# Kernel optimization log

Measured on AMD Instinct MI355X. Metric: run time of the kernel, lower is better.

## Reference

```python
import jax, jax.numpy as jnp
import numpy as np

B, N, D = 128, 64, 2048   # batch, num_slots, slot_dim
M, K, C = 8, 4096, 256    # num_codebooks, codebook_size, code_dim
BLK = D // M              # block size per codebook = 256
COMMIT = 0.25


def setup_inputs() -> dict:
    key = jax.random.key(0)
    ks = jax.random.split(key, 5)
    return {
        "slots": jax.random.normal(ks[0], (B, N, D), dtype=jnp.float32),
        # per-codebook input projections: Linear(BLK -> C), stacked over M
        "Wp": jax.random.normal(ks[1], (M, BLK, C), dtype=jnp.float32) * (1.0 / np.sqrt(BLK)),
        "bp": jnp.zeros((M, C), dtype=jnp.float32),
        # M codebooks of K codes each, uniform(-1/K, 1/K) like the torch init
        "codebooks": jax.random.uniform(ks[2], (M, K, C), dtype=jnp.float32, minval=-1.0 / K, maxval=1.0 / K),
        # per-codebook output projections: Linear(C -> BLK)
        "Wo": jax.random.normal(ks[3], (M, C, BLK), dtype=jnp.float32) * (1.0 / np.sqrt(C)),
        "bo": jnp.zeros((M, BLK), dtype=jnp.float32),
    }


def reference(slots, Wp, bp, codebooks, Wo, bo):
    # split slots into M blocks: [B, N, M, BLK]
    blocks = slots.reshape(B, N, M, BLK)
    # per-codebook projection -> [B, N, M, C]
    x = jnp.einsum('bnmd,mdc->bnmc', blocks, Wp) + bp
    # squared-euclidean distances to each code: [B, N, M, K]
    dist = (jnp.sum(x * x, axis=-1, keepdims=True)
            + jnp.sum(codebooks * codebooks, axis=-1)[None, None]  # [M, K]
            - 2.0 * jnp.einsum('bnmc,mkc->bnmk', x, codebooks))
    idx = jnp.argmin(dist, axis=-1)                 # [B, N, M] int
    # gather codes: codebooks[m, idx[b,n,m]] -> [B, N, M, C]
    q = codebooks[jnp.arange(M)[None, None, :], idx]
    # VQ loss: per-codebook mse summed then / M == global mean over [B,N,M,C]
    q_loss = jnp.mean((q - jax.lax.stop_gradient(x)) ** 2)
    e_loss = jnp.mean((jax.lax.stop_gradient(q) - x) ** 2)
    loss = q_loss + COMMIT * e_loss
    # straight-through estimator
    q_st = x + jax.lax.stop_gradient(q - x)
    # per-codebook output projection and concat of blocks -> [B, N, D]
    out = jnp.einsum('bnmc,mcd->bnmd', q_st, Wo) + bo
    return out.reshape(B, N, D), loss, idx
```

## Files before the change

### kernel.cpp

```cpp
#include <hip/hip_runtime.h>
#include <hip/hip_bf16.h>

typedef float f32x4 __attribute__((ext_vector_type(4)));
typedef float f32x2 __attribute__((ext_vector_type(2)));
typedef short bf16x8 __attribute__((ext_vector_type(8)));

static constexpr size_t WS_LOSSP = 0;
static constexpr size_t WS_UMIN  = 16384;
static constexpr size_t WS_B32   = 294912;
static constexpr size_t WS_IDX   = 425984;
static constexpr size_t WS_CNT   = 688128;
static constexpr size_t WS_LST   = 950272;
static constexpr size_t WS_XH    = 3145728;
static constexpr size_t WS_CBT   = 70254592;

#define DELTA 3.0e-4f

__device__ inline unsigned int fkey(float f) {
  unsigned int b = __float_as_uint(f); return (b & 0x80000000u) ? ~b : (b | 0x80000000u);
}
__device__ inline float funkey(unsigned int u) {
  unsigned int b = (u & 0x80000000u) ? (u ^ 0x80000000u) : ~u; return __uint_as_float(b);
}

__device__ inline f32x2 pk_mul(f32x2 a, f32x2 b) {
  f32x2 d;
  asm("v_pk_mul_f32 %0, %1, %2" : "=v"(d) : "v"(a), "v"(b));
  return d;
}
__device__ inline f32x2 pk_add(f32x2 a, f32x2 b) {
  f32x2 d;
  asm("v_pk_add_f32 %0, %1, %2" : "=v"(d) : "v"(a), "v"(b));
  return d;
}

__device__ inline float np_pw256sq(const float* p, int stride) {
#pragma clang fp contract(off)
  float h2[2];
#pragma unroll
  for (int hh = 0; hh < 2; ++hh) {
    const float* q = p + (size_t)(hh * 128) * stride;
    float V[16];
#pragma unroll
    for (int i = 0; i < 16; ++i) {
      float e[8];
#pragma unroll
      for (int j = 0; j < 8; ++j) { float x = q[(size_t)(j * 16 + i) * stride]; e[j] = x * x; }
      float t01 = e[0] + e[1], t23 = e[2] + e[3], t45 = e[4] + e[5], t67 = e[6] + e[7];
      float ta = t01 + t23, tb = t45 + t67;
      V[i] = ta + tb;
    }
    float u[8];
#pragma unroll
    for (int i = 0; i < 8; ++i) u[i] = V[i] + V[8 + i];
    float w[4];
#pragma unroll
    for (int i = 0; i < 4; ++i) w[i] = u[i] + u[4 + i];
    float wa = w[0] + w[2], wb = w[1] + w[3];
    h2[hh] = wa + wb;
  }
  return h2[0] + h2[1];
}

__global__ __launch_bounds__(256) void k_cbnormB(const float* __restrict__ cb,
                                                 float* __restrict__ B32) {
  int row = blockIdx.x * 256 + threadIdx.x;
  B32[row] = np_pw256sq(cb + (size_t)row * 256, 1);
}

__global__ __launch_bounds__(256) void k_cbb(const float* __restrict__ cb,
                                             unsigned short* __restrict__ cbb) {
  int bx = blockIdx.x;
  int m = bx >> 8, kt = bx & 255;
  const float* src = cb + ((size_t)m * 4096 + kt * 16) * 256;
  unsigned short* dst = cbb + ((size_t)(m * 256 + kt)) * 4096;
  int tid = threadIdx.x;
#pragma unroll
  for (int h = 0; h < 2; ++h) {
    int p = tid + h * 256;
    int cs = p >> 6, lane = p & 63, row = lane & 15, grp = lane >> 4;
    const float* s = src + (size_t)row * 256 + grp * 8 + cs * 32;
    f32x4 v0 = *(const f32x4*)s;
    f32x4 v1 = *(const f32x4*)(s + 4);
    union { unsigned short us[8]; uint4 u; } o;
#pragma unroll
    for (int j = 0; j < 4; ++j) {
      __hip_bfloat16 h0 = __float2bfloat16(v0[j]);
      __hip_bfloat16 h1 = __float2bfloat16(v1[j]);
      o.us[j]     = *reinterpret_cast<unsigned short*>(&h0);
      o.us[4 + j] = *reinterpret_cast<unsigned short*>(&h1);
    }
    *(uint4*)(dst + (size_t)p * 8) = o.u;
  }
}

__global__ __launch_bounds__(256) void k_xhat(const float* __restrict__ slots,
                                              const float* __restrict__ Wp,
                                              const float* __restrict__ bp,
                                              float* __restrict__ XH) {
#pragma clang fp contract(off)
  int bx = blockIdx.x;
  int m = bx & 7, tt = bx >> 3;
  int t0 = tt * 16;
  __shared__ float Ls[16 * 260];
  __shared__ float Wt[16 * 264];
  int tid = threadIdx.x;
  {
#pragma unroll
    for (int i = 0; i < 4; ++i) {
      int f = tid + 256 * i;
      int r = f >> 6, seg = f & 63;
      *(f32x4*)&Ls[r * 260 + seg * 4] =
          *(const f32x4*)(slots + (size_t)(t0 + r) * 2048 + m * 256 + seg * 4);
    }
  }
  int tl = tid & 15, g = tid >> 4;
  const float* lsrow = &Ls[tl * 260];
  const f32x4* wglob = (const f32x4*)(Wp + (size_t)m * 65536);
  f32x4 preg[4];
#pragma unroll
  for (int i = 0; i < 4; ++i) preg[i] = wglob[tid + 256 * i];

  f32x2 acc[8];
#pragma unroll
  for (int i = 0; i < 8; ++i) acc[i] = f32x2{0.f, 0.f};

  for (int chunk = 0; chunk < 16; ++chunk) {
    __syncthreads();
    {
      f32x4* wt4 = (f32x4*)Wt;
#pragma unroll
      for (int i = 0; i < 4; ++i) {
        int q = tid + 256 * i;
        wt4[(q >> 6) * 66 + (q & 63)] = preg[i];
      }
    }
    __syncthreads();
    if (chunk + 1 < 16) {
      const f32x4* src = wglob + (chunk + 1) * 1024;
#pragma unroll
      for (int i = 0; i < 4; ++i) preg[i] = src[tid + 256 * i];
    }
    const float* xs = lsrow + chunk * 16;
#pragma unroll 4
    for (int d = 0; d < 16; ++d) {
      float x = xs[d];
      f32x2 x2 = {x, x};
      const f32x4* wrow = (const f32x4*)&Wt[d * 264 + g * 16];
#pragma unroll
      for (int cq = 0; cq < 4; ++cq) {
        f32x4 wv = wrow[cq];
        f32x2 wlo = {wv[0], wv[1]};
        f32x2 whi = {wv[2], wv[3]};
        acc[cq * 2]     = pk_add(acc[cq * 2],     pk_mul(x2, wlo));
        acc[cq * 2 + 1] = pk_add(acc[cq * 2 + 1], pk_mul(x2, whi));
      }
    }
  }
  int ch0 = g * 16;
  const float* bpb = bp + m * 256 + ch0;
  float* xgbase = XH + (size_t)m * 2097152 + t0 + tl;
#pragma unroll
  for (int i = 0; i < 8; ++i) {
    float v0 = acc[i][0] + bpb[i * 2];
    float v1 = acc[i][1] + bpb[i * 2 + 1];
    xgbase[(size_t)(ch0 + i * 2) * 8192]     = v0;
    xgbase[(size_t)(ch0 + i * 2 + 1) * 8192] = v1;
  }
}

__global__ __launch_bounds__(256, 2) void k_scanA(const float* __restrict__ XH,
                                                  const unsigned short* __restrict__ CBb,
                                                  const float* __restrict__ B32,
                                                  unsigned int* __restrict__ gumin) {
  int bx = blockIdx.x;
  int m = bx & 7, ks = (bx >> 3) & 1, tt = bx >> 4;
  int t0 = tt * 256, kt0 = ks * 128;
  __shared__ unsigned short Bt[3][2 * 4096];
  __shared__ unsigned int umin[256];
  int tid = threadIdx.x;
  umin[tid] = 0xFFFFFFFFu;
  int w = tid >> 6, l = tid & 63;
  int row = l & 15, grp = l >> 4;
  int tbase = w * 64;
  const float FINF = __builtin_inff();

  bf16x8 afrag[4][8];
  {
    const float* xbase = XH + (size_t)m * 2097152;
#pragma unroll
    for (int a = 0; a < 4; ++a)
#pragma unroll
      for (int cs = 0; cs < 8; ++cs) {
        union { short s[8]; bf16x8 v; } u;
#pragma unroll
        for (int j = 0; j < 8; ++j) {
          int c = cs * 32 + grp * 8 + j;
          float x = xbase[(size_t)c * 8192 + t0 + tbase + a * 16 + row];
          __hip_bfloat16 h = __float2bfloat16(x);
          u.s[j] = *reinterpret_cast<short*>(&h);
        }
        afrag[a][cs] = u.v;
      }
  }

  const uint4* cbsrc = (const uint4*)(CBb + (size_t)m * 1048576);
  const float* bvbase = B32 + m * 4096;
  auto stage = [&](int g, int b) {
    const uint4* s = cbsrc + (size_t)(kt0 + 2 * g) * 512;
    uint4* db = (uint4*)Bt[b];
#pragma unroll
    for (int h = 0; h < 4; ++h) {
      int c0 = h * 256 + w * 64;
      __builtin_amdgcn_global_load_lds(
          (const __attribute__((address_space(1))) void*)(s + c0 + l),
          (__attribute__((address_space(3))) void*)(db + c0),
          16, 0, 0);
    }
  };

  float rmin[16];
#pragma unroll
  for (int sl = 0; sl < 16; ++sl) rmin[sl] = FINF;
  stage(0, 0); stage(1, 1);
  asm volatile("s_waitcnt vmcnt(4)" ::: "memory");
  __builtin_amdgcn_s_barrier();
  for (int p = 0; p < 64; ++p) {
    int b = p % 3;
    if (p + 2 < 64) stage(p + 2, (p + 2) % 3);
#pragma unroll
    for (int t = 0; t < 2; ++t) {
      int kt = kt0 + 2 * p + t;
      float Bv = bvbase[kt * 16 + row];
      f32x4 acc[4];
#pragma unroll
      for (int a = 0; a < 4; ++a) acc[a] = f32x4{0.f,0.f,0.f,0.f};
#pragma unroll
      for (int cs = 0; cs < 8; ++cs) {
        bf16x8 bf = *(const bf16x8*)&Bt[b][t * 4096 + cs * 512 + l * 8];
#pragma unroll
        for (int a = 0; a < 4; ++a)
          acc[a] = __builtin_amdgcn_mfma_f32_16x16x32_bf16(afrag[a][cs], bf, acc[a], 0, 0, 0);
      }
#pragma unroll
      for (int a = 0; a < 4; ++a)
#pragma unroll
        for (int r = 0; r < 4; ++r)
          rmin[a * 4 + r] = fminf(rmin[a * 4 + r], fmaf(-2.0f, acc[a][r], Bv));
    }
    if (p < 62) {
      asm volatile("s_waitcnt vmcnt(4)" ::: "memory");
      __builtin_amdgcn_s_barrier();
    } else if (p == 62) {
      asm volatile("s_waitcnt vmcnt(0)" ::: "memory");
      __builtin_amdgcn_s_barrier();
    }
  }
#pragma unroll
  for (int a = 0; a < 4; ++a)
#pragma unroll
    for (int r = 0; r < 4; ++r)
      atomicMin(&umin[tbase + a * 16 + grp * 4 + r], fkey(rmin[a * 4 + r]));
  __syncthreads();
  atomicMin(&gumin[(size_t)(t0 + tid) * 8 + m], umin[tid]);
}

__global__ __launch_bounds__(256, 2) void k_scanB(const float* __restrict__ XH,
                                                  const unsigned short* __restrict__ CBb,
                                                  const float* __restrict__ B32,
                                                  const unsigned int* __restrict__ gumin,
                                                  int* __restrict__ cnts,
                                                  unsigned short* __restrict__ lists) {
  int bx = blockIdx.x;
  int m = bx & 7, ks = (bx >> 3) & 1, tt = bx >> 4;
  int t0 = tt * 256, kt0 = ks * 128;
  __shared__ unsigned short Bt[3][2 * 4096];
  __shared__ int lcnt[256];
  __shared__ unsigned short llist[256][16];
  int tid = threadIdx.x;
  lcnt[tid] = 0;
  int w = tid >> 6, l = tid & 63;
  int row = l & 15, grp = l >> 4;
  int tbase = w * 64;

  bf16x8 afrag[4][8];
  {
    const float* xbase = XH + (size_t)m * 2097152;
#pragma unroll
    for (int a = 0; a < 4; ++a)
#pragma unroll
      for (int cs = 0; cs < 8; ++cs) {
        union { short s[8]; bf16x8 v; } u;
#pragma unroll
        for (int j = 0; j < 8; ++j) {
          int c = cs * 32 + grp * 8 + j;
          float x = xbase[(size_t)c * 8192 + t0 + tbase + a * 16 + row];
          __hip_bfloat16 h = __float2bfloat16(x);
          u.s[j] = *reinterpret_cast<short*>(&h);
        }
        afrag[a][cs] = u.v;
      }
  }
  float thr[16];
#pragma unroll
  for (int a = 0; a < 4; ++a)
#pragma unroll
    for (int r = 0; r < 4; ++r) {
      int tok = t0 + tbase + a * 16 + grp * 4 + r;
      thr[a * 4 + r] = funkey(gumin[(size_t)tok * 8 + m]) + DELTA;
    }

  const uint4* cbsrc = (const uint4*)(CBb + (size_t)m * 1048576);
  const float* bvbase = B32 + m * 4096;
  auto stage = [&](int g, int b) {
    const uint4* s = cbsrc + (size_t)(kt0 + 2 * g) * 512;
    uint4* db = (uint4*)Bt[b];
#pragma unroll
    for (int h = 0; h < 4; ++h) {
      int c0 = h * 256 + w * 64;
      __builtin_amdgcn_global_load_lds(
          (const __attribute__((address_space(1))) void*)(s + c0 + l),
          (__attribute__((address_space(3))) void*)(db + c0),
          16, 0, 0);
    }
  };

  stage(0, 0); stage(1, 1);
  asm volatile("s_waitcnt vmcnt(4)" ::: "memory");
  __builtin_amdgcn_s_barrier();
  for (int p = 0; p < 64; ++p) {
    int b = p % 3;
    if (p + 2 < 64) stage(p + 2, (p + 2) % 3);
#pragma unroll
    for (int t = 0; t < 2; ++t) {
      int kt = kt0 + 2 * p + t;
      float Bv = bvbase[kt * 16 + row];
      f32x4 acc[4];
#pragma unroll
      for (int a = 0; a < 4; ++a) acc[a] = f32x4{0.f,0.f,0.f,0.f};
#pragma unroll
      for (int cs = 0; cs < 8; ++cs) {
        bf16x8 bf = *(const bf16x8*)&Bt[b][t * 4096 + cs * 512 + l * 8];
#pragma unroll
        for (int a = 0; a < 4; ++a)
          acc[a] = __builtin_amdgcn_mfma_f32_16x16x32_bf16(afrag[a][cs], bf, acc[a], 0, 0, 0);
      }
      int k = (kt << 4) + row;
#pragma unroll
      for (int a = 0; a < 4; ++a)
#pragma unroll
        for (int r = 0; r < 4; ++r) {
          float s = fmaf(-2.0f, acc[a][r], Bv);
          if (s <= thr[a * 4 + r]) {
            int tok = tbase + a * 16 + grp * 4 + r;
            int pos = atomicAdd(&lcnt[tok], 1);
            if (pos < 16) llist[tok][pos] = (unsigned short)k;
          }
        }
    }
    if (p < 62) {
      asm volatile("s_waitcnt vmcnt(4)" ::: "memory");
      __builtin_amdgcn_s_barrier();
    } else if (p == 62) {
      asm volatile("s_waitcnt vmcnt(0)" ::: "memory");
      __builtin_amdgcn_s_barrier();
    }
  }
  __syncthreads();
  {
    int n = lcnt[tid];
    if (n > 0) {
      size_t t8m = (size_t)(t0 + tid) * 8 + m;
      int base = atomicAdd(&cnts[t8m], n);
      int nc = n < 16 ? n : 16;
      for (int i = 0; i < nc && base + i < 16; ++i)
        lists[t8m * 16 + base + i] = llist[tid][i];
    }
  }
}

__global__ __launch_bounds__(256) void k_select(const float* __restrict__ XH,
                                                const float* __restrict__ cb,
                                                const float* __restrict__ B32,
                                                const int* __restrict__ cnts,
                                                const unsigned short* __restrict__ lists,
                                                int* __restrict__ idxp) {
#pragma clang fp contract(off)
  int bx = blockIdx.x;
  int m = bx & 7, tt = bx >> 3;
  int t0 = tt * 64;
  __shared__ float XT2[256 * 65];
  __shared__ float Atok[64];
  __shared__ int ovlist[64];
  __shared__ int ovcnt;
  __shared__ float bvD[64];
  __shared__ int bvK[64];
  int tid = threadIdx.x;
  const float* xsrc = XH + (size_t)m * 2097152;
#pragma unroll
  for (int i = 0; i < 16; ++i) {
    int f = tid + 256 * i;
    int c = f >> 4, to = (f & 15) * 4;
    f32x4 v = *(const f32x4*)(xsrc + (size_t)c * 8192 + t0 + to);
    XT2[c*65+to+0]=v[0]; XT2[c*65+to+1]=v[1]; XT2[c*65+to+2]=v[2]; XT2[c*65+to+3]=v[3];
  }
  if (tid == 0) ovcnt = 0;
  __syncthreads();
  if (tid < 64) Atok[tid] = np_pw256sq(&XT2[tid], 65);
  __syncthreads();
  int q = tid >> 2, j = tid & 3;
  const float* cbm = cb + (size_t)m * 1048576;

  auto dist_np = [&](int k, int qq, float A) -> float {
#pragma clang fp contract(off)
    const float* row = cbm + (size_t)k * 256;
    float s = 0.0f;
    for (int i8 = 0; i8 < 256; i8 += 8) {
      float p0 = XT2[(i8 + j) * 65 + qq] * row[i8 + j];
      s = s + p0;
      float p1 = XT2[(i8 + 4 + j) * 65 + qq] * row[i8 + 4 + j];
      s = s + p1;
    }
    float o  = __shfl_xor(s, 1, 64);
    float ts = s + o;
    float o2 = __shfl_xor(ts, 2, 64);
    float red = ts + o2;
    float T1 = A + B32[m * 4096 + k];
    return T1 - 2.0f * red;
  };

  int t8m = (t0 + q) * 8 + m;
  int n = cnts[t8m];
  float A = Atok[q];
  if (n <= 16) {
    float best = __builtin_inff();
    int bk = 0;
    for (int ci = 0; ci < n; ++ci) {
      int k = (int)lists[(size_t)t8m * 16 + ci] & 4095;
      float d2 = dist_np(k, q, A);
      if (d2 < best || (d2 == best && k < bk)) { best = d2; bk = k; }
    }
    if (j == 0) idxp[t8m] = bk;
  } else {
    if (j == 0) { int pos = atomicAdd(&ovcnt, 1); ovlist[pos] = q; }
  }
  __syncthreads();
  int ovn = ovcnt;
  for (int e = 0; e < ovn; ++e) {
    int qq = ovlist[e];
    float Aq = Atok[qq];
    float bd = __builtin_inff(); int bk2 = 0;
    for (int it = 0; it < 64; ++it) {
      int k = it * 64 + q;
      float d2 = dist_np(k, qq, Aq);
      if (d2 < bd) { bd = d2; bk2 = k; }
    }
    if (j == 0) { bvD[q] = bd; bvK[q] = bk2; }
    __syncthreads();
    if (tid == 0) {
      float bb = bvD[0]; int kk2 = bvK[0];
      for (int r = 1; r < 64; ++r) {
        if (bvD[r] < bb || (bvD[r] == bb && bvK[r] < kk2)) { bb = bvD[r]; kk2 = bvK[r]; }
      }
      idxp[(t0 + qq) * 8 + m] = kk2;
    }
    __syncthreads();
  }
}

__global__ __launch_bounds__(256) void k_out(const float* __restrict__ cb,
                                             const float* __restrict__ Wo,
                                             const float* __restrict__ bo,
                                             const float* __restrict__ XH,
                                             const int* __restrict__ idxp,
                                             float* __restrict__ outp,
                                             double* __restrict__ lossp) {
  int bx = blockIdx.x;
  int m = bx & 7, tt = bx >> 3;
  int t0 = tt * 32;
  __shared__ float qT[256 * 32];
  __shared__ float Wl[64 * 256];
  __shared__ double red[256];
  int tid = threadIdx.x;
  {
    int tok = tid & 31, g = tid >> 5;
    int ix = idxp[(size_t)(t0 + tok) * 8 + m] & 4095;
    const float* qrow = cb + ((size_t)m * 4096 + ix) * 256;
#pragma unroll
    for (int i = 0; i < 8; ++i) {
      int c = (g * 8 + i) * 4;
      f32x4 v = *(const f32x4*)(qrow + c);
      qT[(c+0)*32+tok]=v[0]; qT[(c+1)*32+tok]=v[1]; qT[(c+2)*32+tok]=v[2]; qT[(c+3)*32+tok]=v[3];
    }
  }
  int tg = tid & 7, dg = tid >> 3;
  float acc[4][8] = {};
  const float* wbase = Wo + (size_t)m * 65536;
  for (int c4 = 0; c4 < 4; ++c4) {
    __syncthreads();
#pragma unroll
    for (int i = 0; i < 16; ++i) {
      int f = tid + 256 * i;
      int cr = f >> 6, doff = (f & 63) * 4;
      *(f32x4*)&Wl[f * 4] = *(const f32x4*)(wbase + (size_t)(c4 * 64 + cr) * 256 + doff);
    }
    __syncthreads();
#pragma unroll 4
    for (int c = 0; c < 64; ++c) {
      f32x4 q4 = *(const f32x4*)&qT[(c4 * 64 + c) * 32 + tg * 4];
      f32x4 w0 = *(const f32x4*)&Wl[c * 256 + dg * 8];
      f32x4 w1 = *(const f32x4*)&Wl[c * 256 + dg * 8 + 4];
#pragma unroll
      for (int i = 0; i < 4; ++i) {
        acc[i][0]+=q4[i]*w0[0]; acc[i][1]+=q4[i]*w0[1]; acc[i][2]+=q4[i]*w0[2]; acc[i][3]+=q4[i]*w0[3];
        acc[i][4]+=q4[i]*w1[0]; acc[i][5]+=q4[i]*w1[1]; acc[i][6]+=q4[i]*w1[2]; acc[i][7]+=q4[i]*w1[3];
      }
    }
  }
#pragma unroll
  for (int i = 0; i < 4; ++i) {
    int t = t0 + tg * 4 + i;
    f32x4 lo, hi;
#pragma unroll
    for (int jj = 0; jj < 4; ++jj) {
      lo[jj] = acc[i][jj]     + bo[m * 256 + dg * 8 + jj];
      hi[jj] = acc[i][jj + 4] + bo[m * 256 + dg * 8 + 4 + jj];
    }
    float* dst = outp + (size_t)t * 2048 + m * 256 + dg * 8;
    *(f32x4*)(dst)     = lo;
    *(f32x4*)(dst + 4) = hi;
  }
  float lp = 0.0f;
  {
    int ltok = tid & 31, cg2 = tid >> 5;
    const float* xg = XH + (size_t)m * 2097152 + t0 + ltok;
    for (int c = cg2 * 32; c < cg2 * 32 + 32; ++c) {
      float qv = qT[c * 32 + ltok];
      float xv = xg[(size_t)c * 8192];
      float d = qv - xv; lp += d * d;
    }
  }
  red[tid] = (double)lp;
  __syncthreads();
  for (int off = 128; off; off >>= 1) { if (tid < off) red[tid] += red[tid + off]; __syncthreads(); }
  if (tid == 0) lossp[bx] = red[0];
}

__global__ void k_final(const double* __restrict__ lossp, float* __restrict__ outp) {
  __shared__ double red[256];
  int tid = threadIdx.x;
  double s = 0.0;
  for (int i = 0; i < 8; ++i) s += lossp[tid + 256 * i];
  red[tid] = s; __syncthreads();
  for (int off = 128; off; off >>= 1) { if (tid < off) red[tid] += red[tid + off]; __syncthreads(); }
  if (tid == 0) outp[16777216] = (float)(1.25 * red[0] / 16777216.0);
}

__global__ void k_idxout(const int* __restrict__ idxp, float* __restrict__ outp) {
  int i = blockIdx.x * 256 + threadIdx.x;
  outp[16777217 + i] = (float)idxp[i];
}

extern "C" void kernel_launch(void* const* d_in, const int* in_sizes, int n_in,
                              void* d_out, int out_size, void* d_ws, size_t ws_size,
                              hipStream_t stream) {
  (void)in_sizes; (void)n_in; (void)out_size; (void)ws_size;
  const float* slots = (const float*)d_in[0];
  const float* Wp    = (const float*)d_in[1];
  const float* bp    = (const float*)d_in[2];
  const float* cb    = (const float*)d_in[3];
  const float* Wo    = (const float*)d_in[4];
  const float* bo    = (const float*)d_in[5];
  float* outp = (float*)d_out;
  char* ws = (char*)d_ws;
  double*         lossp = (double*)(ws + WS_LOSSP);
  unsigned int*   gumin = (unsigned int*)(ws + WS_UMIN);
  float*          B32   = (float*)(ws + WS_B32);
  int*            idxp  = (int*)(ws + WS_IDX);
  int*            cnts  = (int*)(ws + WS_CNT);
  unsigned short* lists = (unsigned short*)(ws + WS_LST);
  float*          XH    = (float*)(ws + WS_XH);
  unsigned short* CBb   = (unsigned short*)(ws + WS_CBT);

  hipMemsetAsync(gumin, 0xFF, 65536 * sizeof(unsigned int), stream);
  hipMemsetAsync(cnts,  0,    65536 * sizeof(int), stream);
  k_cbnormB<<<128,  256, 0, stream>>>(cb, B32);
  k_cbb    <<<2048, 256, 0, stream>>>(cb, CBb);
  k_xhat   <<<4096, 256, 0, stream>>>(slots, Wp, bp, XH);
  k_scanA  <<<512,  256, 0, stream>>>(XH, CBb, B32, gumin);
  k_scanB  <<<512,  256, 0, stream>>>(XH, CBb, B32, gumin, cnts, lists);
  k_select <<<1024, 256, 0, stream>>>(XH, cb, B32, cnts, lists, idxp);
  k_out    <<<2048, 256, 0, stream>>>(cb, Wo, bo, XH, idxp, outp, lossp);
  k_final  <<<1,    256, 0, stream>>>(lossp, outp);
  k_idxout <<<256,  256, 0, stream>>>(idxp, outp);
}
```

Before: 729.0 us.

## Rewrite output projection as bf16 MFMA with pre-transposed Wo and LDS pipelining

The output projection kernel moves from fp32 FMA to bf16 MFMA 16x16x32. A new kernel pre-converts Wo to bf16 in MFMA fragment order, and tiles of it are streamed into a triple-buffered LDS ring with global_load_lds. Each block now covers 128 tokens instead of 32, and the loss term reads codebook rows directly instead of from shared memory. This cuts FP32 ALU cost in the projection, but rounding codes and weights to bf16 adds error to the output, and the output stores are scattered per element.

```diff
diff --git a/kernel.cpp b/kernel.cpp
--- a/kernel.cpp
+++ b/kernel.cpp
@@ -13,6 +13,7 @@
 static constexpr size_t WS_LST   = 950272;
 static constexpr size_t WS_XH    = 3145728;
 static constexpr size_t WS_CBT   = 70254592;
+static constexpr size_t WS_WOT   = 87031808;
 
 #define DELTA 3.0e-4f
 
@@ -89,6 +90,28 @@
       __hip_bfloat16 h1 = __float2bfloat16(v1[j]);
       o.us[j]     = *reinterpret_cast<unsigned short*>(&h0);
       o.us[4 + j] = *reinterpret_cast<unsigned short*>(&h1);
+    }
+    *(uint4*)(dst + (size_t)p * 8) = o.u;
+  }
+}
+
+__global__ __launch_bounds__(256) void k_wot(const float* __restrict__ Wo,
+                                             unsigned short* __restrict__ wot) {
+  int bx = blockIdx.x;
+  int m = bx >> 4, dt = bx & 15;
+  const float* src = Wo + (size_t)m * 65536 + dt * 16;
+  unsigned short* dst = wot + ((size_t)(m * 16 + dt)) * 4096;
+  int tid = threadIdx.x;
+#pragma unroll
+  for (int h = 0; h < 2; ++h) {
+    int p = tid + h * 256;
+    int cs = p >> 6, lane = p & 63, row = lane & 15, grp = lane >> 4;
+    union { unsigned short us[8]; uint4 u; } o;
+#pragma unroll
+    for (int j = 0; j < 8; ++j) {
+      float v = src[(size_t)(cs * 32 + grp * 8 + j) * 256 + row];
+      __hip_bfloat16 hb = __float2bfloat16(v);
+      o.us[j] = *reinterpret_cast<unsigned short*>(&hb);
     }
     *(uint4*)(dst + (size_t)p * 8) = o.u;
   }
@@ -468,79 +491,101 @@
   }
 }
 
-__global__ __launch_bounds__(256) void k_out(const float* __restrict__ cb,
-                                             const float* __restrict__ Wo,
-                                             const float* __restrict__ bo,
-                                             const float* __restrict__ XH,
-                                             const int* __restrict__ idxp,
-                                             float* __restrict__ outp,
-                                             double* __restrict__ lossp) {
+__global__ __launch_bounds__(256, 2) void k_out(const float* __restrict__ cb,
+                                                const unsigned short* __restrict__ WoT,
+                                                const float* __restrict__ bo,
+                                                const float* __restrict__ XH,
+                                                const int* __restrict__ idxp,
+                                                float* __restrict__ outp,
+                                                double* __restrict__ lossp) {
   int bx = blockIdx.x;
   int m = bx & 7, tt = bx >> 3;
-  int t0 = tt * 32;
-  __shared__ float qT[256 * 32];
-  __shared__ float Wl[64 * 256];
+  int t0 = tt * 128;
+  __shared__ unsigned short Bt[3][4096];
   __shared__ double red[256];
   int tid = threadIdx.x;
+  int w = tid >> 6, l = tid & 63;
+  int row = l & 15, grp = l >> 4;
+  int tw = w * 32;
+
+  bf16x8 afrag[2][8];
+#pragma unroll
+  for (int a = 0; a < 2; ++a) {
+    int tok = t0 + tw + a * 16 + row;
+    int ix = idxp[(size_t)tok * 8 + m] & 4095;
+    const float* qrow = cb + (size_t)m * 1048576 + (size_t)ix * 256;
+#pragma unroll
+    for (int cs = 0; cs < 8; ++cs) {
+      union { short s[8]; bf16x8 v; } u;
+#pragma unroll
+      for (int j = 0; j < 8; ++j) {
+        float v = qrow[cs * 32 + grp * 8 + j];
+        __hip_bfloat16 h = __float2bfloat16(v);
+        u.s[j] = *reinterpret_cast<short*>(&h);
+      }
+      afrag[a][cs] = u.v;
+    }
+  }
+
+  const uint4* wsrc = (const uint4*)(WoT + (size_t)m * 65536);
+  auto stage = [&](int dtile, int b) {
+    const uint4* s = wsrc + (size_t)dtile * 512;
+    uint4* db = (uint4*)Bt[b];
+#pragma unroll
+    for (int h = 0; h < 2; ++h) {
+      int c0 = h * 256 + w * 64;
+      __builtin_amdgcn_global_load_lds(
+          (const __attribute__((address_space(1))) void*)(s + c0 + l),
+          (__attribute__((address_space(3))) void*)(db + c0),
+          16, 0, 0);
+    }
+  };
+
+  stage(0, 0); stage(1, 1);
+  asm volatile("s_waitcnt vmcnt(2)" ::: "memory");
+  __builtin_amdgcn_s_barrier();
+  for (int dt = 0; dt < 16; ++dt) {
+    int b = dt % 3;
+    if (dt + 2 < 16) stage(dt + 2, (dt + 2) % 3);
+    f32x4 acc[2];
+#pragma unroll
+    for (int a = 0; a < 2; ++a) acc[a] = f32x4{0.f,0.f,0.f,0.f};
+#pragma unroll
+    for (int cs = 0; cs < 8; ++cs) {
+      bf16x8 bf = *(const bf16x8*)&Bt[b][cs * 512 + l * 8];
+#pragma unroll
+      for (int a = 0; a < 2; ++a)
+        acc[a] = __builtin_amdgcn_mfma_f32_16x16x32_bf16(afrag[a][cs], bf, acc[a], 0, 0, 0);
+    }
+    float bov = bo[m * 256 + dt * 16 + row];
+#pragma unroll
+    for (int a = 0; a < 2; ++a)
+#pragma unroll
+      for (int r = 0; r < 4; ++r)
+        outp[(size_t)(t0 + tw + a * 16 + grp * 4 + r) * 2048 + m * 256 + dt * 16 + row] =
+            acc[a][r] + bov;
+    if (dt < 14) {
+      asm volatile("s_waitcnt vmcnt(2)" ::: "memory");
+      __builtin_amdgcn_s_barrier();
+    } else if (dt == 14) {
+      asm volatile("s_waitcnt vmcnt(0)" ::: "memory");
+      __builtin_amdgcn_s_barrier();
+    }
+  }
+
   {
-    int tok = tid & 31, g = tid >> 5;
-    int ix = idxp[(size_t)(t0 + tok) * 8 + m] & 4095;
-    const float* qrow = cb + ((size_t)m * 4096 + ix) * 256;
-#pragma unroll
-    for (int i = 0; i < 8; ++i) {
-      int c = (g * 8 + i) * 4;
-      f32x4 v = *(const f32x4*)(qrow + c);
-      qT[(c+0)*32+tok]=v[0]; qT[(c+1)*32+tok]=v[1]; qT[(c+2)*32+tok]=v[2]; qT[(c+3)*32+tok]=v[3];
-    }
-  }
-  int tg = tid & 7, dg = tid >> 3;
-  float acc[4][8] = {};
-  const float* wbase = Wo + (size_t)m * 65536;
-  for (int c4 = 0; c4 < 4; ++c4) {
-    __syncthreads();
-#pragma unroll
-    for (int i = 0; i < 16; ++i) {
-      int f = tid + 256 * i;
-      int cr = f >> 6, doff = (f & 63) * 4;
-      *(f32x4*)&Wl[f * 4] = *(const f32x4*)(wbase + (size_t)(c4 * 64 + cr) * 256 + doff);
-    }
-    __syncthreads();
-#pragma unroll 4
-    for (int c = 0; c < 64; ++c) {
-      f32x4 q4 = *(const f32x4*)&qT[(c4 * 64 + c) * 32 + tg * 4];
-      f32x4 w0 = *(const f32x4*)&Wl[c * 256 + dg * 8];
-      f32x4 w1 = *(const f32x4*)&Wl[c * 256 + dg * 8 + 4];
-#pragma unroll
-      for (int i = 0; i < 4; ++i) {
-        acc[i][0]+=q4[i]*w0[0]; acc[i][1]+=q4[i]*w0[1]; acc[i][2]+=q4[i]*w0[2]; acc[i][3]+=q4[i]*w0[3];
-        acc[i][4]+=q4[i]*w1[0]; acc[i][5]+=q4[i]*w1[1]; acc[i][6]+=q4[i]*w1[2]; acc[i][7]+=q4[i]*w1[3];
-      }
-    }
-  }
-#pragma unroll
-  for (int i = 0; i < 4; ++i) {
-    int t = t0 + tg * 4 + i;
-    f32x4 lo, hi;
-#pragma unroll
-    for (int jj = 0; jj < 4; ++jj) {
-      lo[jj] = acc[i][jj]     + bo[m * 256 + dg * 8 + jj];
-      hi[jj] = acc[i][jj + 4] + bo[m * 256 + dg * 8 + 4 + jj];
-    }
-    float* dst = outp + (size_t)t * 2048 + m * 256 + dg * 8;
-    *(f32x4*)(dst)     = lo;
-    *(f32x4*)(dst + 4) = hi;
-  }
-  float lp = 0.0f;
-  {
-    int ltok = tid & 31, cg2 = tid >> 5;
-    const float* xg = XH + (size_t)m * 2097152 + t0 + ltok;
-    for (int c = cg2 * 32; c < cg2 * 32 + 32; ++c) {
-      float qv = qT[c * 32 + ltok];
-      float xv = xg[(size_t)c * 8192];
-      float d = qv - xv; lp += d * d;
-    }
-  }
-  red[tid] = (double)lp;
+    int tok = tid >> 1, half = tid & 1;
+    int gt = t0 + tok;
+    int ix = idxp[(size_t)gt * 8 + m] & 4095;
+    const float* qrow = cb + (size_t)m * 1048576 + (size_t)ix * 256 + half * 128;
+    const float* xcol = XH + (size_t)m * 2097152 + (size_t)(half * 128) * 8192 + gt;
+    float lp = 0.0f;
+    for (int c = 0; c < 128; ++c) {
+      float d = qrow[c] - xcol[(size_t)c * 8192];
+      lp += d * d;
+    }
+    red[tid] = (double)lp;
+  }
   __syncthreads();
   for (int off = 128; off; off >>= 1) { if (tid < off) red[tid] += red[tid + off]; __syncthreads(); }
   if (tid == 0) lossp[bx] = red[0];
@@ -550,7 +595,7 @@
   __shared__ double red[256];
   int tid = threadIdx.x;
   double s = 0.0;
-  for (int i = 0; i < 8; ++i) s += lossp[tid + 256 * i];
+  for (int i = 0; i < 2; ++i) s += lossp[tid + 256 * i];
   red[tid] = s; __syncthreads();
   for (int off = 128; off; off >>= 1) { if (tid < off) red[tid] += red[tid + off]; __syncthreads(); }
   if (tid == 0) outp[16777216] = (float)(1.25 * red[0] / 16777216.0);
@@ -581,16 +626,18 @@
   unsigned short* lists = (unsigned short*)(ws + WS_LST);
   float*          XH    = (float*)(ws + WS_XH);
   unsigned short* CBb   = (unsigned short*)(ws + WS_CBT);
+  unsigned short* WoTb  = (unsigned short*)(ws + WS_WOT);
 
   hipMemsetAsync(gumin, 0xFF, 65536 * sizeof(unsigned int), stream);
   hipMemsetAsync(cnts,  0,    65536 * sizeof(int), stream);
   k_cbnormB<<<128,  256, 0, stream>>>(cb, B32);
   k_cbb    <<<2048, 256, 0, stream>>>(cb, CBb);
+  k_wot    <<<128,  256, 0, stream>>>(Wo, WoTb);
   k_xhat   <<<4096, 256, 0, stream>>>(slots, Wp, bp, XH);
   k_scanA  <<<512,  256, 0, stream>>>(XH, CBb, B32, gumin);
   k_scanB  <<<512,  256, 0, stream>>>(XH, CBb, B32, gumin, cnts, lists);
   k_select <<<1024, 256, 0, stream>>>(XH, cb, B32, cnts, lists, idxp);
-  k_out    <<<2048, 256, 0, stream>>>(cb, Wo, bo, XH, idxp, outp, lossp);
+  k_out    <<<512,  256, 0, stream>>>(cb, WoTb, bo, XH, idxp, outp, lossp);
   k_final  <<<1,    256, 0, stream>>>(lossp, outp);
   k_idxout <<<256,  256, 0, stream>>>(idxp, outp);
 }
```

Result: faster. 599.0 us, median of 2 (-17.8%).
